# Kernel optimization log

Measured on AMD Instinct MI355X. Metric: run time of the kernel, lower is better.

## Reference

```python
import jax, jax.numpy as jnp
import numpy as np

B, S, H = 2, 256, 2048
HK, HV, DK, DV, K = 16, 32, 128, 128, 4
KEY_DIM = HK * DK          # 2048
VAL_DIM = HV * DV          # 4096
CONV_DIM = 2 * KEY_DIM + VAL_DIM  # 8192
EPS = 1e-6


def setup_inputs() -> dict:
    key = jax.random.key(0)
    ks = jax.random.split(key, 10)
    s = 0.02
    return {
        "hidden_states": jax.random.normal(ks[0], (B, S, H), jnp.float32),
        "conv_state": jnp.zeros((B, CONV_DIM, K - 1), jnp.float32),
        "recurrent_state": jnp.zeros((B, HV, DK, DV), jnp.float32),
        "context_lengths": jnp.full((B,), S, jnp.int32),
        "W_qkv": jax.random.normal(ks[1], (H, CONV_DIM), jnp.float32) * s,
        "W_z": jax.random.normal(ks[2], (H, VAL_DIM), jnp.float32) * s,
        "W_b": jax.random.normal(ks[3], (H, HV), jnp.float32) * s,
        "W_a": jax.random.normal(ks[4], (H, HV), jnp.float32) * s,
        "conv_w": jax.random.normal(ks[5], (CONV_DIM, K), jnp.float32) * 0.1,
        "conv_b": jnp.zeros((CONV_DIM,), jnp.float32),
        "A_log": jax.random.normal(ks[6], (HV,), jnp.float32) * 0.1,
        "dt_bias": jnp.zeros((HV,), jnp.float32),
        "norm_w": jnp.ones((DV,), jnp.float32),
        "W_out": jax.random.normal(ks[7], (VAL_DIM, H), jnp.float32) * s,
    }


def _l2norm(x):
    return x * jax.lax.rsqrt(jnp.sum(x * x, axis=-1, keepdims=True) + EPS)


def reference(hidden_states, conv_state, recurrent_state, context_lengths,
              W_qkv, W_z, W_b, W_a, conv_w, conv_b, A_log, dt_bias,
              norm_w, W_out):
    # input projections
    mixed = hidden_states @ W_qkv            # [B,S,CONV_DIM]
    z = hidden_states @ W_z                  # [B,S,VAL_DIM]
    b = hidden_states @ W_b                  # [B,S,HV]
    a = hidden_states @ W_a                  # [B,S,HV]

    # stateful causal depthwise conv1d (kernel K, padding K-1)
    x_pad = jnp.concatenate([jnp.swapaxes(conv_state, 1, 2), mixed], axis=1)  # [B,S+K-1,C]
    conv_out = conv_b + sum(x_pad[:, j:j + S, :] * conv_w[:, j] for j in range(K))
    conv_state_out = jnp.swapaxes(x_pad[:, S:, :], 1, 2)  # last K-1 raw inputs [B,C,K-1]
    mixed = jax.nn.silu(conv_out)

    q, k, v = jnp.split(mixed, [KEY_DIM, 2 * KEY_DIM], axis=-1)
    q = _l2norm(q.reshape(B, S, HK, DK)) * (DK ** -0.5)
    k = _l2norm(k.reshape(B, S, HK, DK))
    v = v.reshape(B, S, HV, DV)
    # GQA-style repeat of key/query heads to value heads
    rep = HV // HK
    q = jnp.repeat(q, rep, axis=2)           # [B,S,HV,DK]
    k = jnp.repeat(k, rep, axis=2)

    # gating: log-decay g and write strength beta
    g = -jnp.exp(A_log) * jax.nn.softplus(a + dt_bias)  # [B,S,HV]
    beta = jax.nn.sigmoid(b)                            # [B,S,HV]

    # time-major for scan
    qs = jnp.swapaxes(q, 0, 1)   # [S,B,HV,DK]
    ks_ = jnp.swapaxes(k, 0, 1)
    vs = jnp.swapaxes(v, 0, 1)   # [S,B,HV,DV]
    gs = jnp.swapaxes(g, 0, 1)   # [S,B,HV]
    bs = jnp.swapaxes(beta, 0, 1)
    mask = jnp.arange(S)[:, None] < context_lengths[None, :]  # [S,B]

    def step(Sst, inp):
        qt, kt, vt, gt, bt, mt = inp
        Sd = Sst * jnp.exp(gt)[..., None, None]                # decay
        kv = jnp.einsum('bhk,bhkv->bhv', kt, Sd)               # prediction
        delta = (vt - kv) * bt[..., None]                      # delta-rule update
        Snew = Sd + jnp.einsum('bhk,bhv->bhkv', kt, delta)
        ot = jnp.einsum('bhk,bhkv->bhv', qt, Snew)
        Snew = jnp.where(mt[:, None, None, None], Snew, Sst)
        ot = jnp.where(mt[:, None, None], ot, 0.0)
        return Snew, ot

    Sfin, outs = jax.lax.scan(step, recurrent_state, (qs, ks_, vs, gs, bs, mask))
    o = jnp.swapaxes(outs, 0, 1)  # [B,S,HV,DV]

    # gated RMSNorm over value head dim
    o = o * jax.lax.rsqrt(jnp.mean(o * o, axis=-1, keepdims=True) + EPS) * norm_w
    o = o * jax.nn.silu(z.reshape(B, S, HV, DV))
    output = o.reshape(B, S, VAL_DIM) @ W_out
    return output, conv_state_out, Sfin
```

## Files before the change

### kernel.cpp

```cpp
#include <hip/hip_runtime.h>
#include <hip/hip_bf16.h>

#define BB     2
#define SEQ    256
#define HH     2048
#define HKc    16
#define HVc    32
#define DKc    128
#define DVc    128
#define KC     4
#define KEYD   2048
#define VALD   4096
#define CONVD  8192
#define MM     (BB*SEQ)
#define EPSf   1e-6f

typedef __attribute__((ext_vector_type(8))) short short8;
typedef __attribute__((ext_vector_type(4))) short short4v;
typedef __attribute__((ext_vector_type(4))) float floatx4;

__device__ __forceinline__ short f2bf(float f) {
  union { float f; unsigned u; } v; v.f = f;
  unsigned r = v.u + 0x7fffu + ((v.u >> 16) & 1u);
  return (short)(r >> 16);
}

#define PADs 40
__global__ __launch_bounds__(256) void gemm_mfma(
    const float* __restrict__ A, const float* __restrict__ Bw,
    float* __restrict__ C, int M, int N, int Kd, int lda) {
  __shared__ short As[64 * PADs];
  __shared__ short Bs[128 * PADs];
  const int tid = threadIdx.x;
  const int wave = tid >> 6, lane = tid & 63;
  const int wm = (wave >> 1) * 32, wn = (wave & 1) * 64;
  const int bm = blockIdx.y * 64, bn = blockIdx.x * 128;
  floatx4 acc[2][4] = {};
  const int a_kq = tid & 7, a_m0 = tid >> 3;
  const int b_n = tid & 127, b_kh = (tid >> 7) * 8;
  const int fm = lane & 15, fq = (lane >> 4) * 8;
  for (int k0 = 0; k0 < Kd; k0 += 32) {
#pragma unroll
    for (int r = 0; r < 2; ++r) {
      int m = a_m0 + r * 32;
      const float4 f = *(const float4*)(A + (size_t)(bm + m) * lda + k0 + a_kq * 4);
      short4v sv; sv[0] = f2bf(f.x); sv[1] = f2bf(f.y); sv[2] = f2bf(f.z); sv[3] = f2bf(f.w);
      *(short4v*)&As[m * PADs + a_kq * 4] = sv;
    }
#pragma unroll
    for (int r = 0; r < 2; ++r) {
      int kk = b_kh + r * 16;
      short8 s;
#pragma unroll
      for (int j = 0; j < 8; ++j)
        s[j] = f2bf(Bw[(size_t)(k0 + kk + j) * N + bn + b_n]);
      *(short8*)&Bs[b_n * PADs + kk] = s;
    }
    __syncthreads();
    short8 af[2], bfr[4];
#pragma unroll
    for (int i = 0; i < 2; ++i)
      af[i] = *(const short8*)&As[(wm + i * 16 + fm) * PADs + fq];
#pragma unroll
    for (int j = 0; j < 4; ++j)
      bfr[j] = *(const short8*)&Bs[(wn + j * 16 + fm) * PADs + fq];
#pragma unroll
    for (int i = 0; i < 2; ++i)
#pragma unroll
      for (int j = 0; j < 4; ++j)
        acc[i][j] = __builtin_amdgcn_mfma_f32_16x16x32_bf16(af[i], bfr[j], acc[i][j], 0, 0, 0);
    __syncthreads();
  }
  const int cn = lane & 15, cr0 = (lane >> 4) * 4;
#pragma unroll
  for (int i = 0; i < 2; ++i)
#pragma unroll
    for (int j = 0; j < 4; ++j)
#pragma unroll
      for (int r = 0; r < 4; ++r)
        C[(size_t)(bm + wm + i * 16 + cr0 + r) * N + bn + wn + j * 16 + cn] = acc[i][j][r];
}

__global__ __launch_bounds__(256) void proj_ab_kernel(
    const float* __restrict__ hs, const float* __restrict__ Wb,
    const float* __restrict__ Wa, const float* __restrict__ A_log,
    const float* __restrict__ dt_bias, float* __restrict__ g_out,
    float* __restrict__ beta_out) {
  __shared__ float xs[HH];
  __shared__ float part[4][64];
  const int row = blockIdx.x;
  const int t = threadIdx.x;
  for (int i = t; i < HH; i += 256) xs[i] = hs[(size_t)row * HH + i];
  __syncthreads();
  const int j = t & 63;
  const int kc = t >> 6;
  const float* W = (j < 32) ? Wb : Wa;
  const int jj = j & 31;
  float p = 0.f;
  const int k0 = kc * 512;
#pragma unroll 8
  for (int k = k0; k < k0 + 512; ++k) p += xs[k] * W[k * 32 + jj];
  part[kc][j] = p;
  __syncthreads();
  if (t < 64) {
    float dot = part[0][t] + part[1][t] + part[2][t] + part[3][t];
    if (t < 32) {
      beta_out[row * HVc + t] = 1.f / (1.f + expf(-dot));
    } else {
      int h = t - 32;
      float x = dot + dt_bias[h];
      float sp = (x > 20.f) ? x : log1pf(expf(x));
      g_out[row * HVc + h] = -expf(A_log[h]) * sp;
    }
  }
}

#define CCH 16
__global__ __launch_bounds__(256) void conv_par_kernel(
    const float* __restrict__ mixed, const float* __restrict__ conv_state,
    const float* __restrict__ conv_w, const float* __restrict__ conv_b,
    float* __restrict__ cs) {
  const int c = blockIdx.x * 256 + threadIdx.x;
  const int s0 = blockIdx.y * CCH;
  const int b = blockIdx.z;
  const float4 w4 = *(const float4*)&conv_w[c * KC];
  const float bias = conv_b[c];
  float r0, r1, r2;
  if (s0 == 0) {
    size_t sb = (size_t)(b * CONVD + c) * (KC - 1);
    r0 = conv_state[sb + 0]; r1 = conv_state[sb + 1]; r2 = conv_state[sb + 2];
  } else {
    r0 = mixed[((size_t)(b * SEQ + s0 - 3)) * CONVD + c];
    r1 = mixed[((size_t)(b * SEQ + s0 - 2)) * CONVD + c];
    r2 = mixed[((size_t)(b * SEQ + s0 - 1)) * CONVD + c];
  }
#pragma unroll
  for (int s = s0; s < s0 + CCH; ++s) {
    size_t off = ((size_t)(b * SEQ + s)) * CONVD + c;
    float x = mixed[off];
    float acc = bias + r0 * w4.x + r1 * w4.y + r2 * w4.z + x * w4.w;
    cs[off] = acc / (1.f + expf(-acc));
    r0 = r1; r1 = r2; r2 = x;
  }
}

__global__ __launch_bounds__(256) void conv_state_out_kernel(
    const float* __restrict__ mixed, float* __restrict__ out2) {
  int idx = blockIdx.x * 256 + threadIdx.x;
  int t = idx % (KC - 1);
  int c = (idx / (KC - 1)) & (CONVD - 1);
  int b = idx / ((KC - 1) * CONVD);
  out2[idx] = mixed[((size_t)(b * SEQ + SEQ - (KC - 1) + t)) * CONVD + c];
}

__global__ __launch_bounds__(64) void l2norm_kernel(float* __restrict__ cs) {
  int bx = blockIdx.x;
  int which = bx & 1;
  int head = (bx >> 1) & 15;
  int row = bx >> 5;
  int lane = threadIdx.x;
  size_t base = (size_t)row * CONVD + (size_t)which * KEYD + head * DKc;
  float v0 = cs[base + lane];
  float v1 = cs[base + lane + 64];
  float ss = v0 * v0 + v1 * v1;
#pragma unroll
  for (int m = 1; m < 64; m <<= 1) ss += __shfl_xor(ss, m, 64);
  float rn = rsqrtf(ss + EPSf);
  if (!which) rn *= 0.08838834764831845f;
  cs[base + lane] = v0 * rn;
  cs[base + lane + 64] = v1 * rn;
}

#define SCH 8
__global__ __launch_bounds__(64, 2) void scan_kernel(
    const float* __restrict__ cs, const float* __restrict__ g_in,
    const float* __restrict__ beta_in, const float* __restrict__ rs0,
    const int* __restrict__ ctx, float* __restrict__ obuf,
    float* __restrict__ sftmp) {
  const int vg = blockIdx.x, h = blockIdx.y, b = blockIdx.z;
  const int bh = b * HVc + h;
  const int lane = threadIdx.x;
  const int kg = lane >> 2;
  const int c4 = lane & 3;
  const int col = vg * 4 + c4;
  const int khead = h >> 1;
  __shared__ float kl[2][SCH * 128];
  __shared__ float ql[2][SCH * 128];
  __shared__ float vl[2][SCH * 4];
  __shared__ float egl[2][SCH];
  __shared__ float btl[2][SCH];
  float S[8];
#pragma unroll
  for (int i = 0; i < 8; ++i)
    S[i] = rs0[((size_t)bh * DKc + kg * 8 + i) * DVc + col];
  const int cl = ctx[b];
  const size_t qgo = (size_t)khead * DKc;
  const size_t kgo = KEYD + (size_t)khead * DKc;
  const size_t vG = 2 * KEYD + (size_t)h * DVc + vg * 4;
  const size_t obase = ((size_t)bh * 32 + vg) * (SEQ * 4);
  const int r0g = b * SEQ;
  const int kg8 = kg * 8;
  float4 kreg[4], qreg[4], vreg;
  float egr = 0.f, btr = 0.f;
#pragma unroll
  for (int it = 0; it < 4; ++it) {
    int idx = it * 64 + lane, s = idx >> 5, d4 = idx & 31;
    const float* rp = cs + (size_t)(r0g + s) * CONVD;
    kreg[it] = *(const float4*)(rp + kgo + d4 * 4);
    qreg[it] = *(const float4*)(rp + qgo + d4 * 4);
  }
  if (lane < 8)       vreg = *(const float4*)(cs + (size_t)(r0g + lane) * CONVD + vG);
  else if (lane < 16) egr = expf(g_in[(r0g + lane - 8) * HVc + h]);
  else if (lane < 24) btr = beta_in[(r0g + lane - 16) * HVc + h];
#pragma unroll
  for (int it = 0; it < 4; ++it) {
    int idx = it * 64 + lane, s = idx >> 5, d4 = idx & 31;
    *(float4*)&kl[0][s * 128 + d4 * 4] = kreg[it];
    *(float4*)&ql[0][s * 128 + d4 * 4] = qreg[it];
  }
  if (lane < 8)       *(float4*)&vl[0][lane * 4] = vreg;
  else if (lane < 16) egl[0][lane - 8] = egr;
  else if (lane < 24) btl[0][lane - 16] = btr;

  const int NCH = SEQ / SCH;
  for (int c = 0; c < NCH; ++c) {
    const int buf = c & 1;
    if (c + 1 < NCH) {
      const int r1 = r0g + (c + 1) * SCH;
#pragma unroll
      for (int it = 0; it < 4; ++it) {
        int idx = it * 64 + lane, s = idx >> 5, d4 = idx & 31;
        const float* rp = cs + (size_t)(r1 + s) * CONVD;
        kreg[it] = *(const float4*)(rp + kgo + d4 * 4);
        qreg[it] = *(const float4*)(rp + qgo + d4 * 4);
      }
      if (lane < 8)       vreg = *(const float4*)(cs + (size_t)(r1 + lane) * CONVD + vG);
      else if (lane < 16) egr = expf(g_in[(r1 + lane - 8) * HVc + h]);
      else if (lane < 24) btr = beta_in[(r1 + lane - 16) * HVc + h];
    }
    for (int s = 0; s < SCH; ++s) {
      const int sg = c * SCH + s;
      const float eg = egl[buf][s], bt = btl[buf][s];
      const float vv = vl[buf][s * 4 + c4];
      const float4* k4 = (const float4*)&kl[buf][s * 128 + kg8];
      const float4* q4 = (const float4*)&ql[buf][s * 128 + kg8];
      if (sg < cl) {
        const float4 kk0 = k4[0], kk1 = k4[1];
        float a0, a1, a2, a3;
        S[0] *= eg; a0 = kk0.x * S[0];
        S[1] *= eg; a1 = kk0.y * S[1];
        S[2] *= eg; a2 = kk0.z * S[2];
        S[3] *= eg; a3 = kk0.w * S[3];
        S[4] *= eg; a0 += kk1.x * S[4];
        S[5] *= eg; a1 += kk1.y * S[5];
        S[6] *= eg; a2 += kk1.z * S[6];
        S[7] *= eg; a3 += kk1.w * S[7];
        float p = (a0 + a1) + (a2 + a3);
        p += __shfl_xor(p, 4, 64);
        p += __shfl_xor(p, 8, 64);
        p += __shfl_xor(p, 16, 64);
        p += __shfl_xor(p, 32, 64);
        const float delta = (vv - p) * bt;
        const float4 qq0 = q4[0], qq1 = q4[1];
        float o0, o1, o2, o3;
        S[0] += kk0.x * delta; o0 = qq0.x * S[0];
        S[1] += kk0.y * delta; o1 = qq0.y * S[1];
        S[2] += kk0.z * delta; o2 = qq0.z * S[2];
        S[3] += kk0.w * delta; o3 = qq0.w * S[3];
        S[4] += kk1.x * delta; o0 += qq1.x * S[4];
        S[5] += kk1.y * delta; o1 += qq1.y * S[5];
        S[6] += kk1.z * delta; o2 += qq1.z * S[6];
        S[7] += kk1.w * delta; o3 += qq1.w * S[7];
        float o = (o0 + o1) + (o2 + o3);
        o += __shfl_xor(o, 4, 64);
        o += __shfl_xor(o, 8, 64);
        o += __shfl_xor(o, 16, 64);
        o += __shfl_xor(o, 32, 64);
        if (kg == 0) obuf[obase + sg * 4 + c4] = o;
      } else {
        if (kg == 0) obuf[obase + sg * 4 + c4] = 0.f;
      }
    }
    if (c + 1 < NCH) {
      const int nb = buf ^ 1;
#pragma unroll
      for (int it = 0; it < 4; ++it) {
        int idx = it * 64 + lane, s = idx >> 5, d4 = idx & 31;
        *(float4*)&kl[nb][s * 128 + d4 * 4] = kreg[it];
        *(float4*)&ql[nb][s * 128 + d4 * 4] = qreg[it];
      }
      if (lane < 8)       *(float4*)&vl[nb][lane * 4] = vreg;
      else if (lane < 16) egl[nb][lane - 8] = egr;
      else if (lane < 24) btl[nb][lane - 16] = btr;
    }
  }
  const size_t sb = (((size_t)bh * 32 + vg) * DKc + kg8) * 4 + c4;
#pragma unroll
  for (int i = 0; i < 8; ++i)
    sftmp[sb + i * 4] = S[i];
}

__global__ __launch_bounds__(128) void sfin_tr_kernel(
    const float* __restrict__ sftmp, float* __restrict__ out_sf) {
  const int dk = blockIdx.x;
  const int bh = blockIdx.y;
  const int dv = threadIdx.x;
  out_sf[((size_t)bh * DKc + dk) * DVc + dv] =
      sftmp[(((size_t)bh * 32 + (dv >> 2)) * DKc + dk) * 4 + (dv & 3)];
}

__global__ __launch_bounds__(64) void normgate_kernel(
    const float* __restrict__ obuf, float* __restrict__ zbuf,
    const float* __restrict__ norm_w) {
  int bx = blockIdx.x;
  int h = bx & 31;
  int row = bx >> 5;
  int b = row >> 8;
  int s = row & (SEQ - 1);
  int lane = threadIdx.x;
  size_t ob = ((size_t)(b * HVc + h) * 32 + (lane >> 2)) * (SEQ * 4) + s * 4 + (lane & 3);
  size_t zb = (size_t)row * VALD + h * DVc;
  float o0 = obuf[ob];
  float o1 = obuf[ob + 16 * (SEQ * 4)];
  float ss = o0 * o0 + o1 * o1;
#pragma unroll
  for (int m = 1; m < 64; m <<= 1) ss += __shfl_xor(ss, m, 64);
  float rms = rsqrtf(ss * (1.f / 128.f) + EPSf);
  float z0 = zbuf[zb + lane];
  float z1 = zbuf[zb + lane + 64];
  zbuf[zb + lane]      = o0 * rms * norm_w[lane]      * (z0 / (1.f + expf(-z0)));
  zbuf[zb + lane + 64] = o1 * rms * norm_w[lane + 64] * (z1 / (1.f + expf(-z1)));
}

extern "C" void kernel_launch(void* const* d_in, const int* in_sizes, int n_in,
                              void* d_out, int out_size, void* d_ws, size_t ws_size,
                              hipStream_t stream) {
  const float* hs        = (const float*)d_in[0];
  const float* conv_st   = (const float*)d_in[1];
  const float* rec_st    = (const float*)d_in[2];
  const int*   ctx       = (const int*)d_in[3];
  const float* W_qkv     = (const float*)d_in[4];
  const float* W_z       = (const float*)d_in[5];
  const float* W_b       = (const float*)d_in[6];
  const float* W_a       = (const float*)d_in[7];
  const float* conv_w    = (const float*)d_in[8];
  const float* conv_b    = (const float*)d_in[9];
  const float* A_log     = (const float*)d_in[10];
  const float* dt_bias   = (const float*)d_in[11];
  const float* norm_w    = (const float*)d_in[12];
  const float* W_out     = (const float*)d_in[13];

  float* out0   = (float*)d_out;
  float* out_cv = out0 + (size_t)MM * HH;
  float* out_sf = out_cv + (size_t)BB * CONVD * (KC - 1);

  float* mixed = (float*)d_ws;
  float* cs    = mixed + (size_t)MM * CONVD;
  float* zbuf  = cs + (size_t)MM * CONVD;
  float* gbuf  = zbuf + (size_t)MM * VALD;
  float* betab = gbuf + (size_t)MM * HVc;
  float* obuf  = mixed;
  float* sftmp = mixed + (size_t)MM * VALD;

  gemm_mfma<<<dim3(CONVD / 128, MM / 64), 256, 0, stream>>>(hs, W_qkv, mixed, MM, CONVD, HH, HH);
  gemm_mfma<<<dim3(VALD / 128, MM / 64), 256, 0, stream>>>(hs, W_z, zbuf, MM, VALD, HH, HH);
  proj_ab_kernel<<<MM, 256, 0, stream>>>(hs, W_b, W_a, A_log, dt_bias, gbuf, betab);
  conv_par_kernel<<<dim3(CONVD / 256, SEQ / CCH, BB), 256, 0, stream>>>(
      mixed, conv_st, conv_w, conv_b, cs);
  conv_state_out_kernel<<<(BB * CONVD * (KC - 1)) / 256, 256, 0, stream>>>(mixed, out_cv);
  l2norm_kernel<<<MM * HKc * 2, 64, 0, stream>>>(cs);
  scan_kernel<<<dim3(32, HVc, BB), 64, 0, stream>>>(cs, gbuf, betab, rec_st, ctx, obuf, sftmp);
  sfin_tr_kernel<<<dim3(DKc, BB * HVc), 128, 0, stream>>>(sftmp, out_sf);
  normgate_kernel<<<MM * HVc, 64, 0, stream>>>(obuf, zbuf, norm_w);
  gemm_mfma<<<dim3(HH / 128, MM / 64), 256, 0, stream>>>(
      zbuf, W_out, out0, MM, HH, VALD, VALD);
}
```

Baseline: 615.1 us.

## Pre-convert activations and transposed weights to bf16 before MFMA GEMMs

Adds kernels that convert hidden states to bf16 and transpose-convert each weight matrix to a K-contiguous bf16 layout. The GEMM then loads vectorized bf16 tiles with register prefetch of the next k-step, replacing strided scalar weight gathers and in-loop conversion. Normgate writes bf16 output directly for the final projection, and the scan step loop is unrolled. This costs extra conversion passes and workspace aliasing each call.

```diff
diff --git a/kernel.cpp b/kernel.cpp
--- a/kernel.cpp
+++ b/kernel.cpp
@@ -25,9 +25,38 @@
   return (short)(r >> 16);
 }
 
+__global__ __launch_bounds__(256) void trconv_kernel(
+    const float* __restrict__ W, short* __restrict__ Wt, int K, int N) {
+  __shared__ float ls[32][36];
+  const int n0 = blockIdx.x * 32;
+  const int k0 = blockIdx.y * 32;
+  const int t = threadIdx.x;
+  const int r = t >> 3, c4 = (t & 7) * 4;
+  const float4 f = *(const float4*)&W[(size_t)(k0 + r) * N + n0 + c4];
+  ls[r][c4] = f.x; ls[r][c4 + 1] = f.y; ls[r][c4 + 2] = f.z; ls[r][c4 + 3] = f.w;
+  __syncthreads();
+  short4v s;
+  s[0] = f2bf(ls[c4 + 0][r]);
+  s[1] = f2bf(ls[c4 + 1][r]);
+  s[2] = f2bf(ls[c4 + 2][r]);
+  s[3] = f2bf(ls[c4 + 3][r]);
+  *(short4v*)&Wt[(size_t)(n0 + r) * K + k0 + c4] = s;
+}
+
+__global__ __launch_bounds__(256) void f2bf_kernel(
+    const float* __restrict__ in, short* __restrict__ out) {
+  const int i = blockIdx.x * 256 + threadIdx.x;
+  const float4 a = *(const float4*)&in[(size_t)i * 8];
+  const float4 b = *(const float4*)&in[(size_t)i * 8 + 4];
+  short8 s;
+  s[0] = f2bf(a.x); s[1] = f2bf(a.y); s[2] = f2bf(a.z); s[3] = f2bf(a.w);
+  s[4] = f2bf(b.x); s[5] = f2bf(b.y); s[6] = f2bf(b.z); s[7] = f2bf(b.w);
+  *(short8*)&out[(size_t)i * 8] = s;
+}
+
 #define PADs 40
-__global__ __launch_bounds__(256) void gemm_mfma(
-    const float* __restrict__ A, const float* __restrict__ Bw,
+__global__ __launch_bounds__(256) void gemm_bf16(
+    const short* __restrict__ A, const short* __restrict__ Bt,
     float* __restrict__ C, int M, int N, int Kd, int lda) {
   __shared__ short As[64 * PADs];
   __shared__ short Bs[128 * PADs];
@@ -36,27 +65,25 @@
   const int wm = (wave >> 1) * 32, wn = (wave & 1) * 64;
   const int bm = blockIdx.y * 64, bn = blockIdx.x * 128;
   floatx4 acc[2][4] = {};
-  const int a_kq = tid & 7, a_m0 = tid >> 3;
-  const int b_n = tid & 127, b_kh = (tid >> 7) * 8;
+  const int sa_m = tid >> 2;
+  const int sa_k = (tid & 3) * 8;
   const int fm = lane & 15, fq = (lane >> 4) * 8;
+  const short* Ap  = A  + (size_t)(bm + sa_m) * lda + sa_k;
+  const short* Bp0 = Bt + (size_t)(bn + sa_m) * Kd + sa_k;
+  const short* Bp1 = Bt + (size_t)(bn + 64 + sa_m) * Kd + sa_k;
+  short8 pa  = *(const short8*)(Ap);
+  short8 pb0 = *(const short8*)(Bp0);
+  short8 pb1 = *(const short8*)(Bp1);
   for (int k0 = 0; k0 < Kd; k0 += 32) {
-#pragma unroll
-    for (int r = 0; r < 2; ++r) {
-      int m = a_m0 + r * 32;
-      const float4 f = *(const float4*)(A + (size_t)(bm + m) * lda + k0 + a_kq * 4);
-      short4v sv; sv[0] = f2bf(f.x); sv[1] = f2bf(f.y); sv[2] = f2bf(f.z); sv[3] = f2bf(f.w);
-      *(short4v*)&As[m * PADs + a_kq * 4] = sv;
+    *(short8*)&As[sa_m * PADs + sa_k] = pa;
+    *(short8*)&Bs[sa_m * PADs + sa_k] = pb0;
+    *(short8*)&Bs[(64 + sa_m) * PADs + sa_k] = pb1;
+    __syncthreads();
+    if (k0 + 32 < Kd) {
+      pa  = *(const short8*)(Ap + k0 + 32);
+      pb0 = *(const short8*)(Bp0 + k0 + 32);
+      pb1 = *(const short8*)(Bp1 + k0 + 32);
     }
-#pragma unroll
-    for (int r = 0; r < 2; ++r) {
-      int kk = b_kh + r * 16;
-      short8 s;
-#pragma unroll
-      for (int j = 0; j < 8; ++j)
-        s[j] = f2bf(Bw[(size_t)(k0 + kk + j) * N + bn + b_n]);
-      *(short8*)&Bs[b_n * PADs + kk] = s;
-    }
-    __syncthreads();
     short8 af[2], bfr[4];
 #pragma unroll
     for (int i = 0; i < 2; ++i)
@@ -238,6 +265,7 @@
       else if (lane < 16) egr = expf(g_in[(r1 + lane - 8) * HVc + h]);
       else if (lane < 24) btr = beta_in[(r1 + lane - 16) * HVc + h];
     }
+#pragma unroll
     for (int s = 0; s < SCH; ++s) {
       const int sg = c * SCH + s;
       const float eg = egl[buf][s], bt = btl[buf][s];
@@ -310,8 +338,8 @@
 }
 
 __global__ __launch_bounds__(64) void normgate_kernel(
-    const float* __restrict__ obuf, float* __restrict__ zbuf,
-    const float* __restrict__ norm_w) {
+    const float* __restrict__ obuf, const float* __restrict__ zbuf,
+    const float* __restrict__ norm_w, short* __restrict__ o16) {
   int bx = blockIdx.x;
   int h = bx & 31;
   int row = bx >> 5;
@@ -328,8 +356,8 @@
   float rms = rsqrtf(ss * (1.f / 128.f) + EPSf);
   float z0 = zbuf[zb + lane];
   float z1 = zbuf[zb + lane + 64];
-  zbuf[zb + lane]      = o0 * rms * norm_w[lane]      * (z0 / (1.f + expf(-z0)));
-  zbuf[zb + lane + 64] = o1 * rms * norm_w[lane + 64] * (z1 / (1.f + expf(-z1)));
+  o16[zb + lane]      = f2bf(o0 * rms * norm_w[lane]      * (z0 / (1.f + expf(-z0))));
+  o16[zb + lane + 64] = f2bf(o1 * rms * norm_w[lane + 64] * (z1 / (1.f + expf(-z1))));
 }
 
 extern "C" void kernel_launch(void* const* d_in, const int* in_sizes, int n_in,
@@ -354,16 +382,24 @@
   float* out_cv = out0 + (size_t)MM * HH;
   float* out_sf = out_cv + (size_t)BB * CONVD * (KC - 1);
 
-  float* mixed = (float*)d_ws;
-  float* cs    = mixed + (size_t)MM * CONVD;
-  float* zbuf  = cs + (size_t)MM * CONVD;
-  float* gbuf  = zbuf + (size_t)MM * VALD;
+  char*  base  = (char*)d_ws;
+  float* mixed = (float*)base;
+  char*  wtB   = base + (size_t)MM * CONVD * 4;
+  short* wt    = (short*)wtB;
+  float* cs    = (float*)wtB;
+  float* zbuf  = (float*)(wtB + (size_t)MM * CONVD * 4);
+  float* gbuf  = (float*)(wtB + (size_t)CONVD * HH * 2);
   float* betab = gbuf + (size_t)MM * HVc;
+  short* hs16  = (short*)(betab + (size_t)MM * HVc);
+  short* o16   = hs16 + (size_t)MM * HH;
   float* obuf  = mixed;
   float* sftmp = mixed + (size_t)MM * VALD;
 
-  gemm_mfma<<<dim3(CONVD / 128, MM / 64), 256, 0, stream>>>(hs, W_qkv, mixed, MM, CONVD, HH, HH);
-  gemm_mfma<<<dim3(VALD / 128, MM / 64), 256, 0, stream>>>(hs, W_z, zbuf, MM, VALD, HH, HH);
+  f2bf_kernel<<<(MM * HH / 8) / 256, 256, 0, stream>>>(hs, hs16);
+  trconv_kernel<<<dim3(CONVD / 32, HH / 32), 256, 0, stream>>>(W_qkv, wt, HH, CONVD);
+  gemm_bf16<<<dim3(CONVD / 128, MM / 64), 256, 0, stream>>>(hs16, wt, mixed, MM, CONVD, HH, HH);
+  trconv_kernel<<<dim3(VALD / 32, HH / 32), 256, 0, stream>>>(W_z, wt, HH, VALD);
+  gemm_bf16<<<dim3(VALD / 128, MM / 64), 256, 0, stream>>>(hs16, wt, zbuf, MM, VALD, HH, HH);
   proj_ab_kernel<<<MM, 256, 0, stream>>>(hs, W_b, W_a, A_log, dt_bias, gbuf, betab);
   conv_par_kernel<<<dim3(CONVD / 256, SEQ / CCH, BB), 256, 0, stream>>>(
       mixed, conv_st, conv_w, conv_b, cs);
@@ -371,7 +407,7 @@
   l2norm_kernel<<<MM * HKc * 2, 64, 0, stream>>>(cs);
   scan_kernel<<<dim3(32, HVc, BB), 64, 0, stream>>>(cs, gbuf, betab, rec_st, ctx, obuf, sftmp);
   sfin_tr_kernel<<<dim3(DKc, BB * HVc), 128, 0, stream>>>(sftmp, out_sf);
-  normgate_kernel<<<MM * HVc, 64, 0, stream>>>(obuf, zbuf, norm_w);
-  gemm_mfma<<<dim3(HH / 128, MM / 64), 256, 0, stream>>>(
-      zbuf, W_out, out0, MM, HH, VALD, VALD);
-}
+  normgate_kernel<<<MM * HVc, 64, 0, stream>>>(obuf, zbuf, norm_w, o16);
+  trconv_kernel<<<dim3(HH / 32, VALD / 32), 256, 0, stream>>>(W_out, wt, VALD, HH);
+  gemm_bf16<<<dim3(HH / 128, MM / 64), 256, 0, stream>>>(o16, wt, out0, MM, HH, VALD, VALD);
+}
```

Result: faster. 515.3 us (-16.2%).
